# Optimization experiments

Measured on AMD Instinct MI355X. Metric: run time of the kernel, lower is better.

## Reference

```python
import jax, jax.numpy as jnp
import numpy as np

LR = 0.1          # RMSprop learning rate (set_hyper_parameters)
ALPHA = 0.9       # RMSprop decay
ITERATIONS = 5    # SVGD iterations
INV_SIG2 = 1.0    # Gaussian posterior score scale (concrete post_grad)
EPS = 1e-8


def setup_inputs() -> dict:
    key = jax.random.key(0)
    k1, k2 = jax.random.split(key)
    x = jax.random.normal(k1, (8, 2048, 8), dtype=jnp.float32)          # [B, N, D] particles
    observation = jax.random.normal(k2, (8, 8), dtype=jnp.float32)      # [B, D]
    return {"x": x, "observation": observation}


def _svgd(x, observation):
    B, N, D = x.shape
    # median heuristic bandwidth h = median(pairwise dist)^2 / log(N), per batch, no-grad
    sq = jnp.sum((x[:, :, None, :] - x[:, None, :, :]) ** 2, axis=-1)   # [B, N, N]
    med = jnp.median(jnp.sqrt(sq).reshape(B, -1), axis=-1)              # [B]
    h = jax.lax.stop_gradient(med ** 2 / jnp.log(jnp.float32(N)))       # [B]
    inv_N = jnp.float32(1.0 / N)

    def post_grad(xc):
        # Gaussian posterior score: d/dx log N(x; observation, sigma^2 I)
        return (observation[:, None, :] - xc) * INV_SIG2                # [B, N, D]

    def step(carry, _):
        xc, s = carry
        dist = xc[:, :, None, :] - xc[:, None, :, :]                    # [B, i, j, D]
        K = jnp.exp(-jnp.sum(dist ** 2, axis=-1) / h[:, None, None])    # [B, i, j] rbf
        g = post_grad(xc)                                               # [B, j, D]
        # phi_i = (1/N) sum_j [ K_ij * g_j + (2/h)(x_i - x_j) K_ij ]
        phi = inv_N * (jnp.einsum('bij,bjd->bid', K, g)
                       + (2.0 / h)[:, None, None] * jnp.einsum('bij,bijd->bid', K, dist))
        # RMSprop (state update under no_grad in the original)
        s = jax.lax.stop_gradient(ALPHA * s + (1.0 - ALPHA) * phi ** 2)
        xc = xc + LR * phi / (jnp.sqrt(s) + EPS)
        return (xc, s), None

    (x, _), _ = jax.lax.scan(step, (x, jnp.zeros_like(x)), None, length=ITERATIONS)
    return x


def reference(x, observation):
    return _svgd(x, observation)
```

## Files before the change

kernel.cpp:

```cpp
#include <hip/hip_runtime.h>
#include <cstdint>

#define BATCH 8
#define NPART 2048
#define DDIM 8
#define NN (NPART * NPART)

#define MJCHUNK 256
#define SJCHUNK 512

constexpr float LR = 0.1f;
constexpr float ALPHA = 0.9f;
constexpr float EPS = 1e-8f;
constexpr float INV_N = 1.0f / (float)NPART;

typedef float v2f __attribute__((ext_vector_type(2)));
typedef float v4f __attribute__((ext_vector_type(4)));

__global__ __launch_bounds__(256) void init_ws_k(unsigned* __restrict__ hist,
                                                 unsigned* __restrict__ prefix,
                                                 unsigned* __restrict__ rank) {
    const int tid = blockIdx.x * 256 + threadIdx.x;
    if (tid < BATCH * 2 * 256) hist[tid] = 0u;
    if (tid < BATCH * 2) {
        prefix[tid] = 0u;
        rank[tid] = (unsigned)(NN / 2) + (unsigned)(tid & 1);
    }
}

__global__ __launch_bounds__(256) void median_hist_k(const float* __restrict__ x,
                                                     unsigned* __restrict__ hist,
                                                     const unsigned* __restrict__ prefix,
                                                     int shift) {
    __shared__ __align__(16) v4f xs0[MJCHUNK];
    __shared__ __align__(16) v4f xs1[MJCHUNK];
    __shared__ float rs[MJCHUNK];
    __shared__ unsigned lh[256 * 32];

    const int b = blockIdx.x;
    const int tid = threadIdx.x;
    const int lane = tid & 31;
    const int trow = tid >> 5;
    const float* xb = x + (size_t)b * NPART * DDIM;

    const unsigned p0 = prefix[2 * b + 0];
    const unsigned p1 = prefix[2 * b + 1];
    const bool same = (p0 == p1);
    const unsigned mask = (shift == 24) ? 0u : (0xFFFFFFFFu << (shift + 8));

    const int ibase = blockIdx.y * 32 + trow * 4;
    v2f xi[4][4];
    float q[4];
#pragma unroll
    for (int rr = 0; rr < 4; ++rr) {
        const v4f t0 = ((const v4f*)(xb + (size_t)(ibase + rr) * DDIM))[0];
        const v4f t1 = ((const v4f*)(xb + (size_t)(ibase + rr) * DDIM))[1];
        xi[rr][0] = t0.xy; xi[rr][1] = t0.zw;
        xi[rr][2] = t1.xy; xi[rr][3] = t1.zw;
        q[rr] = t0.x * t0.x + t0.y * t0.y + t0.z * t0.z + t0.w * t0.w
              + t1.x * t1.x + t1.y * t1.y + t1.z * t1.z + t1.w * t1.w;
    }

    const int nsel = same ? 1 : 2;
    for (int sel = 0; sel < nsel; ++sel) {
        const unsigned pref = sel ? p1 : p0;
        __syncthreads();
        for (int t = tid; t < 256 * 32; t += 256) lh[t] = 0u;

        for (int cbase = 0; cbase < NPART; cbase += MJCHUNK) {
            __syncthreads();
            for (int t = tid; t < MJCHUNK; t += 256) {
                const v4f u0 = ((const v4f*)(xb + (size_t)(cbase + t) * DDIM))[0];
                const v4f u1 = ((const v4f*)(xb + (size_t)(cbase + t) * DDIM))[1];
                xs0[t] = u0;
                xs1[t] = u1;
                rs[t] = u0.x * u0.x + u0.y * u0.y + u0.z * u0.z + u0.w * u0.w
                      + u1.x * u1.x + u1.y * u1.y + u1.z * u1.z + u1.w * u1.w;
            }
            __syncthreads();
#pragma unroll 2
            for (int j = lane; j < MJCHUNK; j += 32) {
                const v4f A = xs0[j];
                const v4f B = xs1[j];
                const float r = rs[j];
                const v2f A0 = A.xy, A1 = A.zw, B0 = B.xy, B1 = B.zw;
#pragma unroll
                for (int rr = 0; rr < 4; ++rr) {
                    v2f p = A0 * xi[rr][0];
                    p += A1 * xi[rr][1];
                    p += B0 * xi[rr][2];
                    p += B1 * xi[rr][3];
                    const float sq = fmaxf(fmaf(-2.0f, p.x + p.y, q[rr] + r), 0.0f);
                    const unsigned u = __float_as_uint(sq);
                    if ((u & mask) == pref)
                        atomicAdd(&lh[((u >> shift) & 255u) * 32 + lane], 1u);
                }
            }
        }
        __syncthreads();
        unsigned tot = 0;
#pragma unroll
        for (int sct = 0; sct < 32; ++sct) tot += lh[tid * 32 + ((sct + tid) & 31)];
        if (tot) {
            atomicAdd(&hist[b * 512 + sel * 256 + tid], tot);
            if (same) atomicAdd(&hist[b * 512 + 256 + tid], tot);
        }
    }
}

__global__ void median_scan_k(unsigned* __restrict__ hist,
                              unsigned* __restrict__ prefix,
                              unsigned* __restrict__ rank,
                              int shift,
                              float* __restrict__ hpar) {
    __shared__ unsigned selv[16];
    const int t = threadIdx.x;
    if (t < 16) {
        const unsigned r = rank[t];
        const unsigned* hb = hist + t * 256;
        unsigned cum = 0;
        int bin = 0;
        for (; bin < 256; ++bin) {
            const unsigned c = hb[bin];
            if (cum + c >= r) break;
            cum += c;
        }
        if (bin > 255) bin = 255;
        const unsigned np = prefix[t] | ((unsigned)bin << shift);
        prefix[t] = np;
        rank[t] = r - cum;
        selv[t] = np;
    }
    __syncthreads();
    for (int q = t; q < 16 * 256; q += 64) hist[q] = 0u;
    if (shift == 8 && t < BATCH) {
        const float v1 = __uint_as_float(selv[2 * t + 0]);
        const float v2 = __uint_as_float(selv[2 * t + 1]);
        const float med = 0.5f * (sqrtf(v1) + sqrtf(v2));
        const float h = (med * med) / logf((float)NPART);
        hpar[2 * t + 0] = -1.0f / h;
        hpar[2 * t + 1] = 2.0f / h;
    }
}

__global__ __launch_bounds__(256) void svgd_step_k(const float* __restrict__ x_in,
                                                   float* __restrict__ x_out,
                                                   float* __restrict__ s,
                                                   const float* __restrict__ hpar,
                                                   const float* __restrict__ obs,
                                                   int first) {
    __shared__ __align__(16) v4f xs0[SJCHUNK];
    __shared__ __align__(16) v4f xs1[SJCHUNK];
    __shared__ float rs[SJCHUNK];
    __shared__ float part[32][32][9];

    const int b = blockIdx.x;
    const int tid = threadIdx.x;
    const int lane = tid & 31;
    const int trow = tid >> 5;
    const float* xb = x_in + (size_t)b * NPART * DDIM;

    const float nih = hpar[2 * b + 0];
    const float c2 = hpar[2 * b + 1];
    const float cdot = -2.0f * nih;

    const int ibase = blockIdx.y * 32 + trow * 4;
    v2f xi[4][4];
    float q[4];
#pragma unroll
    for (int rr = 0; rr < 4; ++rr) {
        const v4f t0 = ((const v4f*)(xb + (size_t)(ibase + rr) * DDIM))[0];
        const v4f t1 = ((const v4f*)(xb + (size_t)(ibase + rr) * DDIM))[1];
        xi[rr][0] = t0.xy; xi[rr][1] = t0.zw;
        xi[rr][2] = t1.xy; xi[rr][3] = t1.zw;
        q[rr] = nih * (t0.x * t0.x + t0.y * t0.y + t0.z * t0.z + t0.w * t0.w
                     + t1.x * t1.x + t1.y * t1.y + t1.z * t1.z + t1.w * t1.w);
    }

    float S0[4] = {0, 0, 0, 0};
    v2f V[4][4];
#pragma unroll
    for (int rr = 0; rr < 4; ++rr)
#pragma unroll
        for (int k = 0; k < 4; ++k) V[rr][k] = (v2f){0, 0};

    for (int cbase = 0; cbase < NPART; cbase += SJCHUNK) {
        __syncthreads();
        for (int t = tid; t < SJCHUNK; t += 256) {
            const v4f u0 = ((const v4f*)(xb + (size_t)(cbase + t) * DDIM))[0];
            const v4f u1 = ((const v4f*)(xb + (size_t)(cbase + t) * DDIM))[1];
            xs0[t] = u0;
            xs1[t] = u1;
            rs[t] = nih * (u0.x * u0.x + u0.y * u0.y + u0.z * u0.z + u0.w * u0.w
                         + u1.x * u1.x + u1.y * u1.y + u1.z * u1.z + u1.w * u1.w);
        }
        __syncthreads();
#pragma unroll 2
        for (int j = lane; j < SJCHUNK; j += 32) {
            const v4f A = xs0[j];
            const v4f B = xs1[j];
            const float r = rs[j];
            const v2f A0 = A.xy, A1 = A.zw, B0 = B.xy, B1 = B.zw;
#pragma unroll
            for (int rr = 0; rr < 4; ++rr) {
                v2f p = A0 * xi[rr][0];
                p += A1 * xi[rr][1];
                p += B0 * xi[rr][2];
                p += B1 * xi[rr][3];
                const float K = __expf(fmaf(cdot, p.x + p.y, q[rr] + r));
                S0[rr] += K;
                const v2f K2 = {K, K};
                V[rr][0] += A0 * K2;
                V[rr][1] += A1 * K2;
                V[rr][2] += B0 * K2;
                V[rr][3] += B1 * K2;
            }
        }
    }
#pragma unroll
    for (int rr = 0; rr < 4; ++rr) {
        const int row = trow * 4 + rr;
        part[row][lane][0] = S0[rr];
        part[row][lane][1] = V[rr][0].x;
        part[row][lane][2] = V[rr][0].y;
        part[row][lane][3] = V[rr][1].x;
        part[row][lane][4] = V[rr][1].y;
        part[row][lane][5] = V[rr][2].x;
        part[row][lane][6] = V[rr][2].y;
        part[row][lane][7] = V[rr][3].x;
        part[row][lane][8] = V[rr][3].y;
    }
    __syncthreads();

    {
        const int d2i = tid & 7;
        const int r2 = tid >> 3;
        const int i2 = blockIdx.y * 32 + r2;
        float S0t = 0.0f, Vt = 0.0f;
#pragma unroll
        for (int l = 0; l < 32; ++l) {
            S0t += part[r2][l][0];
            Vt += part[r2][l][1 + d2i];
        }
        const size_t idx = ((size_t)b * NPART + i2) * DDIM + d2i;
        const float xid = x_in[idx];
        const float obsd = obs[b * DDIM + d2i];
        const float U = fmaf(S0t, xid, -Vt);
        const float T = fmaf(S0t, obsd - xid, U);
        const float phi = INV_N * fmaf(c2, U, T);
        float sv;
        if (first) {
            sv = (1.0f - ALPHA) * phi * phi;
        } else {
            sv = ALPHA * s[idx] + (1.0f - ALPHA) * phi * phi;
        }
        s[idx] = sv;
        x_out[idx] = xid + LR * phi / (sqrtf(sv) + EPS);
    }
}

extern "C" void kernel_launch(void* const* d_in, const int* in_sizes, int n_in,
                              void* d_out, int out_size, void* d_ws, size_t ws_size,
                              hipStream_t stream) {
    const float* x0 = (const float*)d_in[0];
    const float* obs = (const float*)d_in[1];
    float* out = (float*)d_out;

    float* xa = (float*)d_ws;
    float* s = xa + BATCH * NPART * DDIM;
    unsigned* hist = (unsigned*)(s + BATCH * NPART * DDIM);
    unsigned* prefix = hist + BATCH * 2 * 256;
    unsigned* rank = prefix + BATCH * 2;
    float* hpar = (float*)(rank + BATCH * 2);

    init_ws_k<<<16, 256, 0, stream>>>(hist, prefix, rank);

    for (int r = 0; r < 3; ++r) {
        const int shift = 24 - 8 * r;
        median_hist_k<<<dim3(BATCH, 64), 256, 0, stream>>>(x0, hist, prefix, shift);
        median_scan_k<<<1, 64, 0, stream>>>(hist, prefix, rank, shift, hpar);
    }

    svgd_step_k<<<dim3(BATCH, 64), 256, 0, stream>>>(x0, out, s, hpar, obs, 1);
    svgd_step_k<<<dim3(BATCH, 64), 256, 0, stream>>>(out, xa, s, hpar, obs, 0);
    svgd_step_k<<<dim3(BATCH, 64), 256, 0, stream>>>(xa, out, s, hpar, obs, 0);
    svgd_step_k<<<dim3(BATCH, 64), 256, 0, stream>>>(out, xa, s, hpar, obs, 0);
    svgd_step_k<<<dim3(BATCH, 64), 256, 0, stream>>>(xa, out, s, hpar, obs, 0);
}
```

Measured before the change: 231.0 us.

## Double grid to 16 rows per block, 64-lane j split, exp2 kernel, shuffle reduction

Both the median histogram and SVGD step kernels now give each block 16 rows instead of 32, with 64 lanes splitting the j loop, and launch twice as many blocks. This fills more of the GPU's compute units, since 512 blocks was small for the device. The SVGD kernel folds log2(e) into the bandwidth and calls the hardware exp2 directly. It also reuses one shared buffer for the tile and the partial sums, and reduces partials with wave shuffles before a smaller shared-memory reduction. In exchange, each block reloads the full j range, so redundant global and shared loads of x double.

Result: no change. 227.4 us (-1.6%).

```diff
diff --git a/kernel.cpp b/kernel.cpp
--- a/kernel.cpp
+++ b/kernel.cpp
@@ -6,13 +6,14 @@
 #define DDIM 8
 #define NN (NPART * NPART)
 
-#define MJCHUNK 256
+#define MJCHUNK 128
 #define SJCHUNK 512
 
 constexpr float LR = 0.1f;
 constexpr float ALPHA = 0.9f;
 constexpr float EPS = 1e-8f;
 constexpr float INV_N = 1.0f / (float)NPART;
+constexpr float LOG2E = 1.44269504088896340736f;
 
 typedef float v2f __attribute__((ext_vector_type(2)));
 typedef float v4f __attribute__((ext_vector_type(4)));
@@ -39,8 +40,9 @@
 
     const int b = blockIdx.x;
     const int tid = threadIdx.x;
-    const int lane = tid & 31;
-    const int trow = tid >> 5;
+    const int lane = tid & 63;
+    const int slot = tid & 31;
+    const int trow = tid >> 6;
     const float* xb = x + (size_t)b * NPART * DDIM;
 
     const unsigned p0 = prefix[2 * b + 0];
@@ -48,7 +50,7 @@
     const bool same = (p0 == p1);
     const unsigned mask = (shift == 24) ? 0u : (0xFFFFFFFFu << (shift + 8));
 
-    const int ibase = blockIdx.y * 32 + trow * 4;
+    const int ibase = blockIdx.y * 16 + trow * 4;
     v2f xi[4][4];
     float q[4];
 #pragma unroll
@@ -78,8 +80,8 @@
                       + u1.x * u1.x + u1.y * u1.y + u1.z * u1.z + u1.w * u1.w;
             }
             __syncthreads();
-#pragma unroll 2
-            for (int j = lane; j < MJCHUNK; j += 32) {
+#pragma unroll
+            for (int j = lane; j < MJCHUNK; j += 64) {
                 const v4f A = xs0[j];
                 const v4f B = xs1[j];
                 const float r = rs[j];
@@ -93,7 +95,7 @@
                     const float sq = fmaxf(fmaf(-2.0f, p.x + p.y, q[rr] + r), 0.0f);
                     const unsigned u = __float_as_uint(sq);
                     if ((u & mask) == pref)
-                        atomicAdd(&lh[((u >> shift) & 255u) * 32 + lane], 1u);
+                        atomicAdd(&lh[((u >> shift) & 255u) * 32 + slot], 1u);
                 }
             }
         }
@@ -138,33 +140,34 @@
         const float v2 = __uint_as_float(selv[2 * t + 1]);
         const float med = 0.5f * (sqrtf(v1) + sqrtf(v2));
         const float h = (med * med) / logf((float)NPART);
-        hpar[2 * t + 0] = -1.0f / h;
+        hpar[2 * t + 0] = -LOG2E / h;
         hpar[2 * t + 1] = 2.0f / h;
     }
 }
 
-__global__ __launch_bounds__(256) void svgd_step_k(const float* __restrict__ x_in,
-                                                   float* __restrict__ x_out,
-                                                   float* __restrict__ s,
-                                                   const float* __restrict__ hpar,
-                                                   const float* __restrict__ obs,
-                                                   int first) {
-    __shared__ __align__(16) v4f xs0[SJCHUNK];
-    __shared__ __align__(16) v4f xs1[SJCHUNK];
-    __shared__ float rs[SJCHUNK];
-    __shared__ float part[32][32][9];
+__global__ __launch_bounds__(256, 4) void svgd_step_k(const float* __restrict__ x_in,
+                                                      float* __restrict__ x_out,
+                                                      float* __restrict__ s,
+                                                      const float* __restrict__ hpar,
+                                                      const float* __restrict__ obs,
+                                                      int first) {
+    __shared__ __align__(16) float smem[4608];
+    v4f* xs0 = (v4f*)smem;
+    v4f* xs1 = (v4f*)(smem + 2048);
+    float* rs = smem + 4096;
+    float (*part)[8][9] = (float (*)[8][9])smem;
 
     const int b = blockIdx.x;
     const int tid = threadIdx.x;
-    const int lane = tid & 31;
-    const int trow = tid >> 5;
+    const int lane = tid & 63;
+    const int trow = tid >> 6;
     const float* xb = x_in + (size_t)b * NPART * DDIM;
 
-    const float nih = hpar[2 * b + 0];
+    const float nih2 = hpar[2 * b + 0];
     const float c2 = hpar[2 * b + 1];
-    const float cdot = -2.0f * nih;
-
-    const int ibase = blockIdx.y * 32 + trow * 4;
+    const float cdot2 = -2.0f * nih2;
+
+    const int ibase = blockIdx.y * 16 + trow * 4;
     v2f xi[4][4];
     float q[4];
 #pragma unroll
@@ -173,8 +176,8 @@
         const v4f t1 = ((const v4f*)(xb + (size_t)(ibase + rr) * DDIM))[1];
         xi[rr][0] = t0.xy; xi[rr][1] = t0.zw;
         xi[rr][2] = t1.xy; xi[rr][3] = t1.zw;
-        q[rr] = nih * (t0.x * t0.x + t0.y * t0.y + t0.z * t0.z + t0.w * t0.w
-                     + t1.x * t1.x + t1.y * t1.y + t1.z * t1.z + t1.w * t1.w);
+        q[rr] = nih2 * (t0.x * t0.x + t0.y * t0.y + t0.z * t0.z + t0.w * t0.w
+                      + t1.x * t1.x + t1.y * t1.y + t1.z * t1.z + t1.w * t1.w);
     }
 
     float S0[4] = {0, 0, 0, 0};
@@ -191,12 +194,12 @@
             const v4f u1 = ((const v4f*)(xb + (size_t)(cbase + t) * DDIM))[1];
             xs0[t] = u0;
             xs1[t] = u1;
-            rs[t] = nih * (u0.x * u0.x + u0.y * u0.y + u0.z * u0.z + u0.w * u0.w
-                         + u1.x * u1.x + u1.y * u1.y + u1.z * u1.z + u1.w * u1.w);
+            rs[t] = nih2 * (u0.x * u0.x + u0.y * u0.y + u0.z * u0.z + u0.w * u0.w
+                          + u1.x * u1.x + u1.y * u1.y + u1.z * u1.z + u1.w * u1.w);
         }
         __syncthreads();
 #pragma unroll 2
-        for (int j = lane; j < SJCHUNK; j += 32) {
+        for (int j = lane; j < SJCHUNK; j += 64) {
             const v4f A = xs0[j];
             const v4f B = xs1[j];
             const float r = rs[j];
@@ -207,7 +210,7 @@
                 p += A1 * xi[rr][1];
                 p += B0 * xi[rr][2];
                 p += B1 * xi[rr][3];
-                const float K = __expf(fmaf(cdot, p.x + p.y, q[rr] + r));
+                const float K = __builtin_amdgcn_exp2f(fmaf(cdot2, p.x + p.y, q[rr] + r));
                 S0[rr] += K;
                 const v2f K2 = {K, K};
                 V[rr][0] += A0 * K2;
@@ -217,28 +220,46 @@
             }
         }
     }
+
+    __syncthreads();
 #pragma unroll
     for (int rr = 0; rr < 4; ++rr) {
-        const int row = trow * 4 + rr;
-        part[row][lane][0] = S0[rr];
-        part[row][lane][1] = V[rr][0].x;
-        part[row][lane][2] = V[rr][0].y;
-        part[row][lane][3] = V[rr][1].x;
-        part[row][lane][4] = V[rr][1].y;
-        part[row][lane][5] = V[rr][2].x;
-        part[row][lane][6] = V[rr][2].y;
-        part[row][lane][7] = V[rr][3].x;
-        part[row][lane][8] = V[rr][3].y;
+        float t0 = S0[rr];
+        float t1 = V[rr][0].x, t2 = V[rr][0].y;
+        float t3 = V[rr][1].x, t4 = V[rr][1].y;
+        float t5 = V[rr][2].x, t6 = V[rr][2].y;
+        float t7 = V[rr][3].x, t8 = V[rr][3].y;
+        t0 += __shfl_xor(t0, 32); t0 += __shfl_xor(t0, 16); t0 += __shfl_xor(t0, 8);
+        t1 += __shfl_xor(t1, 32); t1 += __shfl_xor(t1, 16); t1 += __shfl_xor(t1, 8);
+        t2 += __shfl_xor(t2, 32); t2 += __shfl_xor(t2, 16); t2 += __shfl_xor(t2, 8);
+        t3 += __shfl_xor(t3, 32); t3 += __shfl_xor(t3, 16); t3 += __shfl_xor(t3, 8);
+        t4 += __shfl_xor(t4, 32); t4 += __shfl_xor(t4, 16); t4 += __shfl_xor(t4, 8);
+        t5 += __shfl_xor(t5, 32); t5 += __shfl_xor(t5, 16); t5 += __shfl_xor(t5, 8);
+        t6 += __shfl_xor(t6, 32); t6 += __shfl_xor(t6, 16); t6 += __shfl_xor(t6, 8);
+        t7 += __shfl_xor(t7, 32); t7 += __shfl_xor(t7, 16); t7 += __shfl_xor(t7, 8);
+        t8 += __shfl_xor(t8, 32); t8 += __shfl_xor(t8, 16); t8 += __shfl_xor(t8, 8);
+        if (lane < 8) {
+            const int row = trow * 4 + rr;
+            part[row][lane][0] = t0;
+            part[row][lane][1] = t1;
+            part[row][lane][2] = t2;
+            part[row][lane][3] = t3;
+            part[row][lane][4] = t4;
+            part[row][lane][5] = t5;
+            part[row][lane][6] = t6;
+            part[row][lane][7] = t7;
+            part[row][lane][8] = t8;
+        }
     }
     __syncthreads();
 
-    {
+    if (tid < 128) {
         const int d2i = tid & 7;
         const int r2 = tid >> 3;
-        const int i2 = blockIdx.y * 32 + r2;
+        const int i2 = blockIdx.y * 16 + r2;
         float S0t = 0.0f, Vt = 0.0f;
 #pragma unroll
-        for (int l = 0; l < 32; ++l) {
+        for (int l = 0; l < 8; ++l) {
             S0t += part[r2][l][0];
             Vt += part[r2][l][1 + d2i];
         }
@@ -277,13 +298,13 @@
 
     for (int r = 0; r < 3; ++r) {
         const int shift = 24 - 8 * r;
-        median_hist_k<<<dim3(BATCH, 64), 256, 0, stream>>>(x0, hist, prefix, shift);
+        median_hist_k<<<dim3(BATCH, 128), 256, 0, stream>>>(x0, hist, prefix, shift);
         median_scan_k<<<1, 64, 0, stream>>>(hist, prefix, rank, shift, hpar);
     }
 
-    svgd_step_k<<<dim3(BATCH, 64), 256, 0, stream>>>(x0, out, s, hpar, obs, 1);
-    svgd_step_k<<<dim3(BATCH, 64), 256, 0, stream>>>(out, xa, s, hpar, obs, 0);
-    svgd_step_k<<<dim3(BATCH, 64), 256, 0, stream>>>(xa, out, s, hpar, obs, 0);
-    svgd_step_k<<<dim3(BATCH, 64), 256, 0, stream>>>(out, xa, s, hpar, obs, 0);
-    svgd_step_k<<<dim3(BATCH, 64), 256, 0, stream>>>(xa, out, s, hpar, obs, 0);
-}
+    svgd_step_k<<<dim3(BATCH, 128), 256, 0, stream>>>(x0, out, s, hpar, obs, 1);
+    svgd_step_k<<<dim3(BATCH, 128), 256, 0, stream>>>(out, xa, s, hpar, obs, 0);
+    svgd_step_k<<<dim3(BATCH, 128), 256, 0, stream>>>(xa, out, s, hpar, obs, 0);
+    svgd_step_k<<<dim3(BATCH, 128), 256, 0, stream>>>(out, xa, s, hpar, obs, 0);
+    svgd_step_k<<<dim3(BATCH, 128), 256, 0, stream>>>(xa, out, s, hpar, obs, 0);
+}
```
